# Performance work log

Measured on AMD Instinct MI355X. Metric: run time of the kernel, lower is better.

The kernel has to match this reference:

```python
import jax, jax.numpy as jnp
import numpy as np
from jax import lax

B, T, R, D = 32, 128, 9, 512


def conv2d(x, w, b):
    # x: (N,C,H,W), w: (O,I,kh,kw)
    y = lax.conv_general_dilated(x, w, (1, 1), 'VALID', dimension_numbers=('NCHW', 'OIHW', 'NCHW'))
    return y + b[None, :, None, None]


def pad1(x):
    return jnp.pad(x, ((0, 0), (0, 0), (1, 1), (1, 1)))


def maxpool2(x):
    return lax.reduce_window(x, -jnp.inf, lax.max, (1, 1, 2, 2), (1, 1, 2, 2), 'VALID')


def f2f_similarity(q, t, qm, tm):
    # q,t: (B,T,R,D). Region-pairwise sims then Chamfer: max over target regions p (axis 3), mean over query regions o (axis 2).
    sim = jnp.einsum('biok,bjpk->biopj', q, t)   # (B,T,R,R,T) large intermediate
    sim = jnp.mean(jnp.max(sim, axis=3), axis=2)  # (B,T,T)
    smask = qm[:, :, None] * tm[:, None, :]       # (B,T,T)
    sim = jnp.where(smask > 0, sim, 0.0)
    return sim, smask


def visil_head(sim, mask, w1, b1, w2, b2, w3, b3, wf, bf):
    # ViSiL VideoComperator: zeropad1+conv3x3+relu+maxpool2 (x2), zeropad1+conv3x3+relu, 1x1 conv
    x = sim[:, None]   # (N,1,T,T)
    m = mask[:, None]
    x = maxpool2(jax.nn.relu(conv2d(pad1(x), w1, b1)))
    m = maxpool2(m)
    x = maxpool2(jax.nn.relu(conv2d(pad1(x), w2, b2)))
    m = maxpool2(m)
    x = jax.nn.relu(conv2d(pad1(x), w3, b3))
    x = conv2d(x, wf, bf)   # 1x1 conv -> 1 channel
    return x[:, 0], m[:, 0]


def chamfer_v2v(s, m):
    # masked Chamfer: max over axis 2, masked mean over axis 1
    s = jnp.where(m > 0, s, -jnp.inf)
    s = jnp.max(s, axis=2)
    mm = jnp.max(m, axis=2)
    s = jnp.where(mm > 0, s, 0.0)
    return jnp.sum(s, axis=1) / jnp.sum(mm, axis=1)


def setup_inputs():
    key = jax.random.key(0)
    ks = jax.random.split(key, 8)
    return {
        'anchors': jax.random.normal(ks[0], (B, T, R, D), jnp.float32),
        'positives': jax.random.normal(ks[1], (B, T, R, D), jnp.float32),
        'negatives': jax.random.normal(ks[2], (B, T, R, D), jnp.float32),
        'anchors_masks': jnp.ones((B, T), jnp.float32),
        'positive_masks': jnp.ones((B, T), jnp.float32),
        'negative_masks': jnp.ones((B, T), jnp.float32),
        'w1': jax.random.normal(ks[3], (32, 1, 3, 3), jnp.float32) * 0.05,
        'b1': jnp.zeros((32,), jnp.float32),
        'w2': jax.random.normal(ks[4], (64, 32, 3, 3), jnp.float32) * 0.05,
        'b2': jnp.zeros((64,), jnp.float32),
        'w3': jax.random.normal(ks[5], (128, 64, 3, 3), jnp.float32) * 0.05,
        'b3': jnp.zeros((128,), jnp.float32),
        'wf': jax.random.normal(ks[6], (1, 128, 1, 1), jnp.float32) * 0.05,
        'bf': jnp.zeros((1,), jnp.float32),
    }


def reference(anchors, positives, negatives, anchors_masks, positive_masks, negative_masks, w1, b1, w2, b2, w3, b3, wf, bf):
    pos_sim, pos_mask = f2f_similarity(anchors, positives, anchors_masks, positive_masks)
    neg_sim, neg_mask = f2f_similarity(anchors, negatives, anchors_masks, negative_masks)
    sim = jnp.concatenate([pos_sim, neg_sim], 0)
    smask = jnp.concatenate([pos_mask, neg_mask], 0)
    sim, smask = visil_head(sim, smask, w1, b1, w2, b2, w3, b3, wf, bf)
    # SimilarityRegularizationLoss(min_val=-1, max_val=1)
    loss = jnp.sum(jax.nn.relu(-1.0 - sim)) + jnp.sum(jax.nn.relu(sim - 1.0))
    sim = jnp.clip(sim, -1.0, 1.0)  # Hardtanh
    v2v = chamfer_v2v(sim, smask)   # (2B,)
    pos_pair, neg_pair = jnp.split(v2v[:, None], 2, axis=0)
    return pos_pair, neg_pair, loss
```

## Files before the change

### kernel.cpp

```cpp
#include <hip/hip_runtime.h>
#include <math.h>

#define BTRD (128*9*512)

typedef _Float16 half8 __attribute__((ext_vector_type(8)));
typedef float f32x4 __attribute__((ext_vector_type(4)));

__global__ __launch_bounds__(256) void prep_kernel(
    const float* __restrict__ P, const float* __restrict__ Nn,
    _Float16* __restrict__ Pf, _Float16* __restrict__ Nf,
    const float* __restrict__ w2, const float* __restrict__ w3,
    _Float16* __restrict__ w2t, _Float16* __restrict__ w3t)
{
  int bid = blockIdx.x;
  if (bid < 18432) {
    int which = bid / 9216;
    const float* in = which == 0 ? P : Nn;
    _Float16* out = which == 0 ? Pf : Nf;
    int idx = (bid - which * 9216) * 256 + threadIdx.x;
    const float4* in4 = (const float4*)in;
    float4 a = in4[idx * 2], c = in4[idx * 2 + 1];
    half8 h = { (_Float16)a.x, (_Float16)a.y, (_Float16)a.z, (_Float16)a.w,
                (_Float16)c.x, (_Float16)c.y, (_Float16)c.z, (_Float16)c.w };
    ((half8*)out)[idx] = h;
  } else {
    int idx = (bid - 18432) * 256 + threadIdx.x;
    if (idx < 18432) {
      int tap = idx >> 11, oc = (idx >> 5) & 63, ic = idx & 31;
      w2t[idx] = (_Float16)w2[(oc * 32 + ic) * 9 + tap];
    } else if (idx < 18432 + 73728) {
      int j = idx - 18432;
      int tap = j >> 13, oc = (j >> 6) & 127, ic = j & 63;
      w3t[j] = (_Float16)w3[(oc * 64 + ic) * 9 + tap];
    }
  }
}

template<int O, int OB>
__device__ __forceinline__ void sim_run(
    const float* __restrict__ Q32, const _Float16* __restrict__ TP,
    const _Float16* __restrict__ TN,
    _Float16* __restrict__ lds, int i0, int tid, int jq, int b,
    const float* __restrict__ qm, const float* __restrict__ pm,
    const float* __restrict__ nm, float* __restrict__ simout)
{
  int lane = tid & 63;
  int lrow = lane & 15, lk8 = lane >> 4;
  _Float16* tb0 = lds + 73728;
  _Float16* tb1 = lds + 73728 + 4096;

  {
    const float* qb = Q32 + ((size_t)(i0 * 9) << 9);
#pragma unroll
    for (int it = 0; it < 18; it++) {
      int c = it * 512 + tid;
      int r = c >> 6, sp = c & 63;
      const float* src = qb + ((size_t)r << 9) + (sp << 3);
      float4 a = *(const float4*)src;
      float4 cc = *(const float4*)(src + 4);
      half8 h = { (_Float16)a.x, (_Float16)a.y, (_Float16)a.z, (_Float16)a.w,
                  (_Float16)cc.x, (_Float16)cc.y, (_Float16)cc.z, (_Float16)cc.w };
      *(half8*)&lds[r * 512 + ((sp ^ (r & 7)) << 3)] = h;
    }
  }
  __syncthreads();

  int jc = tid >> 2, spc = tid & 3;
  int ld = jc * 32 + ((spc ^ ((jc >> 1) & 3)) << 3);

  float* ex = (float*)(lds + 73728);
  const float* qmv = qm + b * 128;
  const float inv9 = 1.0f / 9.0f;

  for (int tsel = 0; tsel < 2; ++tsel) {
    const _Float16* tg = (tsel ? TN : TP) + (size_t)jc * 4608 + (spc << 3);

    half8 st[4];
    f32x4 acc[O][2], mx[O][2];
#pragma unroll
    for (int oo = 0; oo < O; oo++)
#pragma unroll
      for (int jt = 0; jt < 2; jt++) {
        acc[oo][jt] = (f32x4){0.f, 0.f, 0.f, 0.f};
        mx[oo][jt] = (f32x4){-INFINITY, -INFINITY, -INFINITY, -INFINITY};
      }

#define T_ISSUE(SET, S) do {                                              \
      int _s = (S);                                                       \
      int _p = _s >> 4; if (_p > 8) _p = 8;                               \
      st[SET] = *(const half8*)(tg + (_p << 9) + ((_s & 15) << 5));       \
    } while (0)

#define T_WRITE(SET, PAR) do {                                            \
      _Float16* _b = (PAR) ? tb1 : tb0;                                   \
      *(half8*)&_b[ld] = st[SET];                                         \
    } while (0)

    T_ISSUE(0, 0);
    T_ISSUE(1, 1);
    T_ISSUE(2, 2);
    T_WRITE(0, 0);
    asm volatile("s_waitcnt lgkmcnt(0)" ::: "memory");
    __builtin_amdgcn_s_barrier();
    __builtin_amdgcn_sched_barrier(0);

    for (int p = 0; p < 9; ++p) {
#pragma unroll
      for (int kc = 0; kc < 16; ++kc) {
        int s = p * 16 + kc;
        T_ISSUE((kc + 3) & 3, s + 3);
        T_WRITE((kc + 1) & 3, (kc + 1) & 1);

        const _Float16* cur = (kc & 1) ? tb1 : tb0;
        half8 bfr[2];
#pragma unroll
        for (int jt = 0; jt < 2; jt++) {
          int j = jq * 32 + jt * 16 + lrow;
          bfr[jt] = *(const half8*)&cur[j * 32 + ((lk8 ^ ((j >> 1) & 3)) << 3)];
        }
#pragma unroll
        for (int oo = 0; oo < O; ++oo) {
          int r = lrow * 9 + OB + oo;
          half8 afr = *(const half8*)&lds[r * 512 + ((((kc << 2) + lk8) ^ (r & 7)) << 3)];
          acc[oo][0] = __builtin_amdgcn_mfma_f32_16x16x32_f16(afr, bfr[0], acc[oo][0], 0, 0, 0);
          acc[oo][1] = __builtin_amdgcn_mfma_f32_16x16x32_f16(afr, bfr[1], acc[oo][1], 0, 0, 0);
        }

        if (kc == 15) {
#pragma unroll
          for (int oo = 0; oo < O; oo++)
#pragma unroll
            for (int jt = 0; jt < 2; jt++) {
#pragma unroll
              for (int e = 0; e < 4; e++)
                mx[oo][jt][e] = fmaxf(mx[oo][jt][e], acc[oo][jt][e]);
              acc[oo][jt] = (f32x4){0.f, 0.f, 0.f, 0.f};
            }
        }
        asm volatile("s_waitcnt lgkmcnt(0)" ::: "memory");
        __builtin_amdgcn_s_barrier();
        __builtin_amdgcn_sched_barrier(0);
      }
    }
#undef T_ISSUE
#undef T_WRITE

    f32x4 ps[2];
#pragma unroll
    for (int jt = 0; jt < 2; jt++) {
      ps[jt] = mx[0][jt];
#pragma unroll
      for (int oo = 1; oo < O; oo++) ps[jt] += mx[oo][jt];
    }

    if (OB != 0) {
#pragma unroll
      for (int jt = 0; jt < 2; jt++)
        *(f32x4*)&ex[((jq * 64 + lane) * 2 + jt) * 4] = ps[jt];
    }
    __syncthreads();
    if (OB == 0) {
      const float* tm = (tsel ? nm : pm) + b * 128;
      int pb = b + tsel * 32;
#pragma unroll
      for (int jt = 0; jt < 2; jt++) {
        ps[jt] += *(const f32x4*)&ex[((jq * 64 + lane) * 2 + jt) * 4];
        int j = jq * 32 + jt * 16 + lrow;
        float tmv = tm[j];
#pragma unroll
        for (int e = 0; e < 4; e++) {
          int i = i0 + (lk8 << 2) + e;
          float m = qmv[i] * tmv;
          simout[((size_t)pb << 14) + (i << 7) + j] = (m > 0.f) ? ps[jt][e] * inv9 : 0.f;
        }
      }
    }
    __syncthreads();
  }
}

__global__ __launch_bounds__(512, 1) void sim_mfma_kernel(
    const float* __restrict__ A32, const _Float16* __restrict__ Pf,
    const _Float16* __restrict__ Nf,
    const float* __restrict__ qm, const float* __restrict__ pm,
    const float* __restrict__ nm, float* __restrict__ simout)
{
  __shared__ _Float16 lds[81920];

  int n = blockIdx.x;
  int xcd = n & 7, slot = n >> 3;
  int b = xcd * 4 + (slot >> 3);
  int ib = slot & 7;
  const float* Q32 = A32 + (size_t)b * BTRD;
  const _Float16* TP = Pf + (size_t)b * BTRD;
  const _Float16* TN = Nf + (size_t)b * BTRD;
  int i0 = ib * 16;

  int tid = threadIdx.x;
  int w = tid >> 6;
  int jq = w & 3;
  if ((w >> 2) == 0)
    sim_run<5, 0>(Q32, TP, TN, lds, i0, tid, jq, b, qm, pm, nm, simout);
  else
    sim_run<4, 5>(Q32, TP, TN, lds, i0, tid, jq, b, qm, pm, nm, simout);
}

__global__ __launch_bounds__(256) void conv1_kernel(
    const float* __restrict__ sim, const float* __restrict__ w1,
    const float* __restrict__ b1, _Float16* __restrict__ x1)
{
  __shared__ float w_s[288];
  __shared__ float b_s[32];
  int tid = threadIdx.x;
  for (int e = tid; e < 288; e += 256) w_s[e] = w1[e];
  if (tid < 32) b_s[tid] = b1[tid];
  __syncthreads();

  int idx = blockIdx.x * 256 + tid;
  int x = idx & 63, y = (idx >> 6) & 63, b2 = idx >> 12;
  const float* sb = sim + (size_t)b2 * 16384;

  float patch[4][4];
#pragma unroll
  for (int r = 0; r < 4; r++) {
    int Y = 2 * y - 1 + r;
#pragma unroll
    for (int c = 0; c < 4; c++) {
      int X = 2 * x - 1 + c;
      patch[r][c] = (Y >= 0 && Y < 128 && X >= 0 && X < 128) ? sb[Y * 128 + X] : 0.f;
    }
  }

  _Float16 vout[32];
#pragma unroll
  for (int oc = 0; oc < 32; oc++) {
    float c00 = 0, c01 = 0, c10 = 0, c11 = 0;
#pragma unroll
    for (int tap = 0; tap < 9; tap++) {
      int dy = tap / 3, dx = tap - dy * 3;
      float w = w_s[oc * 9 + tap];
      c00 = fmaf(w, patch[dy][dx], c00);
      c01 = fmaf(w, patch[dy][dx + 1], c01);
      c10 = fmaf(w, patch[dy + 1][dx], c10);
      c11 = fmaf(w, patch[dy + 1][dx + 1], c11);
    }
    float v = fmaxf(fmaxf(c00, c01), fmaxf(c10, c11)) + b_s[oc];
    vout[oc] = (_Float16)fmaxf(v, 0.f);
  }
  _Float16* dst = x1 + (((size_t)b2 * 64 + y) * 64 + x) * 32;
#pragma unroll
  for (int q = 0; q < 4; q++)
    *(half8*)(dst + q * 8) = *(half8*)&vout[q * 8];
}

__global__ __launch_bounds__(256, 2) void conv2_mfma(
    const _Float16* __restrict__ x1, const _Float16* __restrict__ w2t,
    const float* __restrict__ bb, _Float16* __restrict__ x2)
{
  __shared__ _Float16 in_s[4 * 6 * 66 * 8];
  __shared__ _Float16 w_s[9 * 64 * 40];
  __shared__ _Float16 pool_s[4][32 * 32];

  int b2 = blockIdx.y, ystrip = blockIdx.x;
  int y0 = ystrip * 4;
  int tid = threadIdx.x;
  int w = tid >> 6, lane = tid & 63;
  int wyp = w >> 1, wn = w & 1;
  int lrow = lane & 15, lk8 = lane >> 4;

  {
    int px = tid >> 2, seg = tid & 3;
    const _Float16* base = x1 + ((size_t)b2 * 64) * 64 * 32;
    for (int rr = 0; rr < 6; rr++) {
      int yy = y0 - 1 + rr;
      half8 v = {};
      if (yy >= 0 && yy < 64) v = *(const half8*)(base + ((size_t)yy * 64 + px) * 32 + seg * 8);
      *(half8*)&in_s[((seg * 6 + rr) * 66 + px + 1) * 8] = v;
    }
    if (tid < 48) {
      int pr = tid >> 1, side = tid & 1;
      *(half8*)&in_s[(pr * 66 + side * 65) * 8] = (half8){};
    }
  }
  for (int e = tid; e < 2304; e += 256)
    *(half8*)&w_s[(e >> 2) * 40 + (e & 3) * 8] = *(const half8*)&w2t[e * 8];
  __syncthreads();

  f32x4 acc[2][4][2];
#pragma unroll
  for (int yr = 0; yr < 2; yr++)
#pragma unroll
    for (int xt = 0; xt < 4; xt++)
#pragma unroll
      for (int nt = 0; nt < 2; nt++)
        acc[yr][xt][nt] = (f32x4){0.f, 0.f, 0.f, 0.f};

#pragma unroll
  for (int tap = 0; tap < 9; tap++) {
    int dy = tap / 3, dx = tap - dy * 3;
    half8 bfr[2];
#pragma unroll
    for (int nt = 0; nt < 2; nt++)
      bfr[nt] = *(const half8*)&w_s[(tap * 64 + wn * 32 + nt * 16 + lrow) * 40 + lk8 * 8];
#pragma unroll
    for (int yr = 0; yr < 2; yr++) {
      int rr = 2 * wyp + yr + dy;
#pragma unroll
      for (int xt = 0; xt < 4; xt++) {
        half8 afr = *(const half8*)&in_s[((lk8 * 6 + rr) * 66 + xt * 16 + lrow + dx) * 8];
#pragma unroll
        for (int nt = 0; nt < 2; nt++)
          acc[yr][xt][nt] = __builtin_amdgcn_mfma_f32_16x16x32_f16(afr, bfr[nt], acc[yr][xt][nt], 0, 0, 0);
      }
    }
  }

  float bbv[2] = { bb[wn * 32 + lrow], bb[wn * 32 + 16 + lrow] };
#pragma unroll
  for (int nt = 0; nt < 2; nt++)
#pragma unroll
    for (int xt = 0; xt < 4; xt++)
#pragma unroll
      for (int pe = 0; pe < 2; pe++) {
        float m = fmaxf(fmaxf(acc[0][xt][nt][2 * pe], acc[0][xt][nt][2 * pe + 1]),
                        fmaxf(acc[1][xt][nt][2 * pe], acc[1][xt][nt][2 * pe + 1]));
        float v = fmaxf(m + bbv[nt], 0.f);
        int px = xt * 8 + lk8 * 2 + pe;
        pool_s[w][px * 32 + nt * 16 + lrow] = (_Float16)v;
      }
  __syncthreads();

  {
    int py = ystrip * 2 + wyp;
    int px = lane & 31, half = lane >> 5;
    const _Float16* srcp = &pool_s[w][px * 32 + half * 16];
    _Float16* dst = x2 + (((size_t)b2 * 32 + py) * 32 + px) * 64 + wn * 32 + half * 16;
    *(half8*)dst = *(const half8*)srcp;
    *(half8*)(dst + 8) = *(const half8*)(srcp + 8);
  }
}

__global__ __launch_bounds__(256, 2) void conv3_mfma(
    const _Float16* __restrict__ x2, const _Float16* __restrict__ w3t,
    const float* __restrict__ b3, const float* __restrict__ wf,
    const float* __restrict__ bf, float* __restrict__ shead)
{
  __shared__ _Float16 in_s[8 * 6 * 34 * 8];
  __shared__ _Float16 w_s[9 * 32 * 72];

  int b2 = blockIdx.y, ystrip = blockIdx.x;
  int y0 = ystrip * 4;
  int tid = threadIdx.x, w = tid >> 6, lane = tid & 63;
  int lrow = lane & 15, lk8 = lane >> 4;

  {
    int px = tid >> 3, seg = tid & 7;
    const _Float16* base = x2 + ((size_t)b2 * 32) * 32 * 64;
    for (int rr = 0; rr < 6; rr++) {
      int yy = y0 - 1 + rr;
      half8 v = {};
      if (yy >= 0 && yy < 32) v = *(const half8*)(base + ((size_t)yy * 32 + px) * 64 + seg * 8);
      *(half8*)&in_s[((seg * 6 + rr) * 34 + px + 1) * 8] = v;
    }
    if (tid < 96) {
      int pr = tid >> 1, side = tid & 1;
      *(half8*)&in_s[(pr * 34 + side * 33) * 8] = (half8){};
    }
  }

  f32x4 spart[2];
  spart[0] = (f32x4){0.f, 0.f, 0.f, 0.f};
  spart[1] = (f32x4){0.f, 0.f, 0.f, 0.f};
  int y = y0 + w;

  for (int og = 0; og < 4; og++) {
    __syncthreads();
    for (int e = tid; e < 2304; e += 256) {
      int s = e & 7, o = (e >> 3) & 31, tap = e >> 8;
      *(half8*)&w_s[(tap * 32 + o) * 72 + s * 8] =
          *(const half8*)&w3t[((size_t)(tap * 128 + og * 32 + o)) * 64 + s * 8];
    }
    __syncthreads();

    f32x4 acc[2][2];
#pragma unroll
    for (int mt = 0; mt < 2; mt++)
#pragma unroll
      for (int nt = 0; nt < 2; nt++)
        acc[mt][nt] = (f32x4){0.f, 0.f, 0.f, 0.f};

#pragma unroll
    for (int tap = 0; tap < 9; tap++) {
      int dy = tap / 3, dx = tap - dy * 3;
#pragma unroll
      for (int kc = 0; kc < 2; kc++) {
        half8 bfr[2];
#pragma unroll
        for (int nt = 0; nt < 2; nt++)
          bfr[nt] = *(const half8*)&w_s[(tap * 32 + nt * 16 + lrow) * 72 + kc * 32 + lk8 * 8];
#pragma unroll
        for (int mt = 0; mt < 2; mt++) {
          half8 afr = *(const half8*)&in_s[(((kc * 4 + lk8) * 6 + w + dy) * 34 + mt * 16 + lrow + dx) * 8];
#pragma unroll
          for (int nt = 0; nt < 2; nt++)
            acc[mt][nt] = __builtin_amdgcn_mfma_f32_16x16x32_f16(afr, bfr[nt], acc[mt][nt], 0, 0, 0);
        }
      }
    }

#pragma unroll
    for (int nt = 0; nt < 2; nt++) {
      int oc = og * 32 + nt * 16 + lrow;
      float b3v = b3[oc], wfv = wf[oc];
#pragma unroll
      for (int mt = 0; mt < 2; mt++)
#pragma unroll
        for (int e = 0; e < 4; e++)
          spart[mt][e] = fmaf(fmaxf(acc[mt][nt][e] + b3v, 0.f), wfv, spart[mt][e]);
    }
  }

#pragma unroll
  for (int mt = 0; mt < 2; mt++)
#pragma unroll
    for (int e = 0; e < 4; e++) {
      float v = spart[mt][e];
      v += __shfl_xor(v, 1); v += __shfl_xor(v, 2);
      v += __shfl_xor(v, 4); v += __shfl_xor(v, 8);
      spart[mt][e] = v;
    }
  if (lrow == 0) {
    float bfv = bf[0];
#pragma unroll
    for (int mt = 0; mt < 2; mt++)
#pragma unroll
      for (int e = 0; e < 4; e++) {
        int x = mt * 16 + lk8 * 4 + e;
        shead[(size_t)b2 * 1024 + y * 32 + x] = spart[mt][e] + bfv;
      }
  }
}

__global__ __launch_bounds__(256) void head_final_kernel(
    const float* __restrict__ shead, const float* __restrict__ qm,
    const float* __restrict__ pm, const float* __restrict__ nm,
    float* __restrict__ out, float* __restrict__ loss_ws)
{
  int b2 = blockIdx.x, b = b2 & 31, g = b2 >> 5;
  const float* qmv = qm + b * 128;
  const float* tmv = (g ? nm : pm) + b * 128;

  __shared__ float mq4[32], mt4[32];
  __shared__ float red[256];
  __shared__ float rowv[32], rowm[32];

  int tid = threadIdx.x;
  if (tid < 32) {
    float a = qmv[tid * 4];
    a = fmaxf(a, qmv[tid * 4 + 1]); a = fmaxf(a, qmv[tid * 4 + 2]); a = fmaxf(a, qmv[tid * 4 + 3]);
    mq4[tid] = a;
    float c = tmv[tid * 4];
    c = fmaxf(c, tmv[tid * 4 + 1]); c = fmaxf(c, tmv[tid * 4 + 2]); c = fmaxf(c, tmv[tid * 4 + 3]);
    mt4[tid] = c;
  }
  __syncthreads();

  const float* s = shead + (size_t)b2 * 1024;
  float lp = 0.f;
#pragma unroll
  for (int r = 0; r < 4; r++) {
    float v = s[tid + 256 * r];
    lp += fmaxf(-1.f - v, 0.f) + fmaxf(v - 1.f, 0.f);
  }
  red[tid] = lp;
  __syncthreads();
  for (int off = 128; off; off >>= 1) {
    if (tid < off) red[tid] += red[tid + off];
    __syncthreads();
  }
  if (tid == 0) loss_ws[b2] = red[0];

  if (tid < 32) {
    int y = tid;
    float mqy = mq4[y];
    float rmax = -INFINITY, mm = 0.f;
    for (int x = 0; x < 32; x++) {
      float m = mqy * mt4[x];
      mm = fmaxf(mm, m);
      float v = s[y * 32 + x];
      v = fminf(fmaxf(v, -1.f), 1.f);
      rmax = fmaxf(rmax, m > 0.f ? v : -INFINITY);
    }
    rowv[y] = (mm > 0.f) ? rmax : 0.f;
    rowm[y] = mm;
  }
  __syncthreads();
  if (tid == 0) {
    float ss = 0.f, sm = 0.f;
    for (int y = 0; y < 32; y++) { ss += rowv[y]; sm += rowm[y]; }
    out[b2] = ss / sm;
  }
}

__global__ void loss_sum_kernel(const float* __restrict__ loss_ws, float* __restrict__ out)
{
  float v = loss_ws[threadIdx.x];
#pragma unroll
  for (int off = 32; off >= 1; off >>= 1) v += __shfl_down(v, off);
  if (threadIdx.x == 0) out[64] = v;
}

extern "C" void kernel_launch(void* const* d_in, const int* in_sizes, int n_in,
                              void* d_out, int out_size, void* d_ws, size_t ws_size,
                              hipStream_t stream)
{
  (void)in_sizes; (void)n_in; (void)out_size; (void)ws_size;
  const float* A   = (const float*)d_in[0];
  const float* P   = (const float*)d_in[1];
  const float* Nn  = (const float*)d_in[2];
  const float* qm  = (const float*)d_in[3];
  const float* pm  = (const float*)d_in[4];
  const float* nm  = (const float*)d_in[5];
  const float* w1  = (const float*)d_in[6];
  const float* b1  = (const float*)d_in[7];
  const float* w2  = (const float*)d_in[8];
  const float* b2w = (const float*)d_in[9];
  const float* w3  = (const float*)d_in[10];
  const float* b3  = (const float*)d_in[11];
  const float* wf  = (const float*)d_in[12];
  const float* bf  = (const float*)d_in[13];
  float* out = (float*)d_out;

  const size_t F16SZ = (size_t)BTRD * 32 * sizeof(_Float16);
  char* ws = (char*)d_ws;
  _Float16* Pf = (_Float16*)(ws);
  _Float16* Nf = (_Float16*)(ws + F16SZ);
  char* ws2 = ws + 2 * F16SZ;
  float*     sim   = (float*)(ws2);
  _Float16*  x1    = (_Float16*)(ws2 + (4u << 20));
  _Float16*  x2    = (_Float16*)(ws2 + (20u << 20));
  float*     shead = (float*)(ws2 + (28u << 20));
  _Float16*  w2t   = (_Float16*)(ws2 + (29u << 20));
  _Float16*  w3t   = (_Float16*)(ws2 + (29u << 20) + (256u << 10));
  float*     lws   = (float*)(ws2 + (30u << 20));

  prep_kernel<<<18792, 256, 0, stream>>>(P, Nn, Pf, Nf, w2, w3, w2t, w3t);

  sim_mfma_kernel<<<256, 512, 0, stream>>>(A, Pf, Nf, qm, pm, nm, sim);
  conv1_kernel<<<1024, 256, 0, stream>>>(sim, w1, b1, x1);
  conv2_mfma<<<dim3(16, 64), 256, 0, stream>>>(x1, w2t, b2w, x2);
  conv3_mfma<<<dim3(8, 64), 256, 0, stream>>>(x2, w3t, b3, wf, bf, shead);
  head_final_kernel<<<64, 256, 0, stream>>>(shead, qm, pm, nm, out, lws);
  loss_sum_kernel<<<1, 64, 0, stream>>>(lws, out);
}
```

Measured before the change: 202.1 us.

## Fuse fp32-to-fp16 conversion of targets into sim kernel and prioritize MFMA waves

Removes the separate prep pass that converted the positive and negative tensors to fp16 in workspace. The sim kernel now loads fp32 target tiles straight from the inputs and converts them to fp16 while staging into LDS. This drops a full read-convert-write round trip over both tensors but doubles the global bytes each sim block loads for targets and adds register pressure. It also raises wave priority with s_setprio around the MFMA section.

```diff
diff --git a/kernel.cpp b/kernel.cpp
--- a/kernel.cpp
+++ b/kernel.cpp
@@ -7,39 +7,24 @@
 typedef float f32x4 __attribute__((ext_vector_type(4)));
 
 __global__ __launch_bounds__(256) void prep_kernel(
-    const float* __restrict__ P, const float* __restrict__ Nn,
-    _Float16* __restrict__ Pf, _Float16* __restrict__ Nf,
     const float* __restrict__ w2, const float* __restrict__ w3,
     _Float16* __restrict__ w2t, _Float16* __restrict__ w3t)
 {
-  int bid = blockIdx.x;
-  if (bid < 18432) {
-    int which = bid / 9216;
-    const float* in = which == 0 ? P : Nn;
-    _Float16* out = which == 0 ? Pf : Nf;
-    int idx = (bid - which * 9216) * 256 + threadIdx.x;
-    const float4* in4 = (const float4*)in;
-    float4 a = in4[idx * 2], c = in4[idx * 2 + 1];
-    half8 h = { (_Float16)a.x, (_Float16)a.y, (_Float16)a.z, (_Float16)a.w,
-                (_Float16)c.x, (_Float16)c.y, (_Float16)c.z, (_Float16)c.w };
-    ((half8*)out)[idx] = h;
-  } else {
-    int idx = (bid - 18432) * 256 + threadIdx.x;
-    if (idx < 18432) {
-      int tap = idx >> 11, oc = (idx >> 5) & 63, ic = idx & 31;
-      w2t[idx] = (_Float16)w2[(oc * 32 + ic) * 9 + tap];
-    } else if (idx < 18432 + 73728) {
-      int j = idx - 18432;
-      int tap = j >> 13, oc = (j >> 6) & 127, ic = j & 63;
-      w3t[j] = (_Float16)w3[(oc * 64 + ic) * 9 + tap];
-    }
+  int idx = blockIdx.x * 256 + threadIdx.x;
+  if (idx < 18432) {
+    int tap = idx >> 11, oc = (idx >> 5) & 63, ic = idx & 31;
+    w2t[idx] = (_Float16)w2[(oc * 32 + ic) * 9 + tap];
+  } else if (idx < 18432 + 73728) {
+    int j = idx - 18432;
+    int tap = j >> 13, oc = (j >> 6) & 127, ic = j & 63;
+    w3t[j] = (_Float16)w3[(oc * 64 + ic) * 9 + tap];
   }
 }
 
 template<int O, int OB>
 __device__ __forceinline__ void sim_run(
-    const float* __restrict__ Q32, const _Float16* __restrict__ TP,
-    const _Float16* __restrict__ TN,
+    const float* __restrict__ Q32, const float* __restrict__ TP,
+    const float* __restrict__ TN,
     _Float16* __restrict__ lds, int i0, int tid, int jq, int b,
     const float* __restrict__ qm, const float* __restrict__ pm,
     const float* __restrict__ nm, float* __restrict__ simout)
@@ -73,9 +58,9 @@
   const float inv9 = 1.0f / 9.0f;
 
   for (int tsel = 0; tsel < 2; ++tsel) {
-    const _Float16* tg = (tsel ? TN : TP) + (size_t)jc * 4608 + (spc << 3);
-
-    half8 st[4];
+    const float* tg = (tsel ? TN : TP) + (size_t)jc * 4608 + (spc << 3);
+
+    float4 sta[4], stb[4];
     f32x4 acc[O][2], mx[O][2];
 #pragma unroll
     for (int oo = 0; oo < O; oo++)
@@ -88,12 +73,18 @@
 #define T_ISSUE(SET, S) do {                                              \
       int _s = (S);                                                       \
       int _p = _s >> 4; if (_p > 8) _p = 8;                               \
-      st[SET] = *(const half8*)(tg + (_p << 9) + ((_s & 15) << 5));       \
+      const float* _src = tg + (_p << 9) + ((_s & 15) << 5);              \
+      sta[SET] = *(const float4*)_src;                                    \
+      stb[SET] = *(const float4*)(_src + 4);                              \
     } while (0)
 
 #define T_WRITE(SET, PAR) do {                                            \
       _Float16* _b = (PAR) ? tb1 : tb0;                                   \
-      *(half8*)&_b[ld] = st[SET];                                         \
+      half8 _h = { (_Float16)sta[SET].x, (_Float16)sta[SET].y,            \
+                   (_Float16)sta[SET].z, (_Float16)sta[SET].w,            \
+                   (_Float16)stb[SET].x, (_Float16)stb[SET].y,            \
+                   (_Float16)stb[SET].z, (_Float16)stb[SET].w };          \
+      *(half8*)&_b[ld] = _h;                                              \
     } while (0)
 
     T_ISSUE(0, 0);
@@ -118,6 +109,7 @@
           int j = jq * 32 + jt * 16 + lrow;
           bfr[jt] = *(const half8*)&cur[j * 32 + ((lk8 ^ ((j >> 1) & 3)) << 3)];
         }
+        __builtin_amdgcn_s_setprio(1);
 #pragma unroll
         for (int oo = 0; oo < O; ++oo) {
           int r = lrow * 9 + OB + oo;
@@ -125,6 +117,7 @@
           acc[oo][0] = __builtin_amdgcn_mfma_f32_16x16x32_f16(afr, bfr[0], acc[oo][0], 0, 0, 0);
           acc[oo][1] = __builtin_amdgcn_mfma_f32_16x16x32_f16(afr, bfr[1], acc[oo][1], 0, 0, 0);
         }
+        __builtin_amdgcn_s_setprio(0);
 
         if (kc == 15) {
 #pragma unroll
@@ -180,8 +173,8 @@
 }
 
 __global__ __launch_bounds__(512, 1) void sim_mfma_kernel(
-    const float* __restrict__ A32, const _Float16* __restrict__ Pf,
-    const _Float16* __restrict__ Nf,
+    const float* __restrict__ A32, const float* __restrict__ P32,
+    const float* __restrict__ N32,
     const float* __restrict__ qm, const float* __restrict__ pm,
     const float* __restrict__ nm, float* __restrict__ simout)
 {
@@ -192,8 +185,8 @@
   int b = xcd * 4 + (slot >> 3);
   int ib = slot & 7;
   const float* Q32 = A32 + (size_t)b * BTRD;
-  const _Float16* TP = Pf + (size_t)b * BTRD;
-  const _Float16* TN = Nf + (size_t)b * BTRD;
+  const float* TP = P32 + (size_t)b * BTRD;
+  const float* TN = N32 + (size_t)b * BTRD;
   int i0 = ib * 16;
 
   int tid = threadIdx.x;
@@ -531,22 +524,18 @@
   const float* bf  = (const float*)d_in[13];
   float* out = (float*)d_out;
 
-  const size_t F16SZ = (size_t)BTRD * 32 * sizeof(_Float16);
   char* ws = (char*)d_ws;
-  _Float16* Pf = (_Float16*)(ws);
-  _Float16* Nf = (_Float16*)(ws + F16SZ);
-  char* ws2 = ws + 2 * F16SZ;
-  float*     sim   = (float*)(ws2);
-  _Float16*  x1    = (_Float16*)(ws2 + (4u << 20));
-  _Float16*  x2    = (_Float16*)(ws2 + (20u << 20));
-  float*     shead = (float*)(ws2 + (28u << 20));
-  _Float16*  w2t   = (_Float16*)(ws2 + (29u << 20));
-  _Float16*  w3t   = (_Float16*)(ws2 + (29u << 20) + (256u << 10));
-  float*     lws   = (float*)(ws2 + (30u << 20));
-
-  prep_kernel<<<18792, 256, 0, stream>>>(P, Nn, Pf, Nf, w2, w3, w2t, w3t);
-
-  sim_mfma_kernel<<<256, 512, 0, stream>>>(A, Pf, Nf, qm, pm, nm, sim);
+  float*     sim   = (float*)(ws);
+  _Float16*  x1    = (_Float16*)(ws + (4u << 20));
+  _Float16*  x2    = (_Float16*)(ws + (20u << 20));
+  float*     shead = (float*)(ws + (28u << 20));
+  _Float16*  w2t   = (_Float16*)(ws + (29u << 20));
+  _Float16*  w3t   = (_Float16*)(ws + (29u << 20) + (256u << 10));
+  float*     lws   = (float*)(ws + (30u << 20));
+
+  prep_kernel<<<360, 256, 0, stream>>>(w2, w3, w2t, w3t);
+
+  sim_mfma_kernel<<<256, 512, 0, stream>>>(A, P, Nn, qm, pm, nm, sim);
   conv1_kernel<<<1024, 256, 0, stream>>>(sim, w1, b1, x1);
   conv2_mfma<<<dim3(16, 64), 256, 0, stream>>>(x1, w2t, b2w, x2);
   conv3_mfma<<<dim3(8, 64), 256, 0, stream>>>(x2, w3t, b3, wf, bf, shead);
```

Result: slower. 290.3 us (+43.6%).

## Stream target tiles directly to LDS with global_load_lds double buffering

Applied to the files above, without the earlier changes.

Replaces the register-staged global-load-then-LDS-store pipeline for target tiles with direct global-to-LDS loads (global_load_lds, 16 bytes), moving the swizzle into the global source address. Each step issues the next tile and waits with vmcnt(1), bracketed by two barriers. This drops register staging and the separate ds_write, but shortens the prefetch distance from three stages to one and adds an extra barrier per step, so global latency may be less hidden.

```diff
diff --git a/kernel.cpp b/kernel.cpp
--- a/kernel.cpp
+++ b/kernel.cpp
@@ -5,6 +5,12 @@
 
 typedef _Float16 half8 __attribute__((ext_vector_type(8)));
 typedef float f32x4 __attribute__((ext_vector_type(4)));
+
+__device__ __forceinline__ void gload16(const _Float16* g, const _Float16* l) {
+  __builtin_amdgcn_global_load_lds(
+      (const __attribute__((address_space(1))) void*)g,
+      (__attribute__((address_space(3))) void*)l, 16, 0, 0);
+}
 
 __global__ __launch_bounds__(256) void prep_kernel(
     const float* __restrict__ P, const float* __restrict__ Nn,
@@ -66,16 +72,16 @@
   __syncthreads();
 
   int jc = tid >> 2, spc = tid & 3;
-  int ld = jc * 32 + ((spc ^ ((jc >> 1) & 3)) << 3);
+  int spl = spc ^ ((jc >> 1) & 3);
+  int wb8 = (tid & ~63) * 8;
 
   float* ex = (float*)(lds + 73728);
   const float* qmv = qm + b * 128;
   const float inv9 = 1.0f / 9.0f;
 
   for (int tsel = 0; tsel < 2; ++tsel) {
-    const _Float16* tg = (tsel ? TN : TP) + (size_t)jc * 4608 + (spc << 3);
-
-    half8 st[4];
+    const _Float16* tg = (tsel ? TN : TP) + (size_t)jc * 4608 + (spl << 3);
+
     f32x4 acc[O][2], mx[O][2];
 #pragma unroll
     for (int oo = 0; oo < O; oo++)
@@ -85,31 +91,28 @@
         mx[oo][jt] = (f32x4){-INFINITY, -INFINITY, -INFINITY, -INFINITY};
       }
 
-#define T_ISSUE(SET, S) do {                                              \
+#define T_ISSUE_G(S) do {                                                 \
       int _s = (S);                                                       \
-      int _p = _s >> 4; if (_p > 8) _p = 8;                               \
-      st[SET] = *(const half8*)(tg + (_p << 9) + ((_s & 15) << 5));       \
+      int _p = _s >> 4;                                                   \
+      _Float16* _buf = ((_s) & 1) ? tb1 : tb0;                            \
+      gload16(tg + (_p << 9) + ((_s & 15) << 5), _buf + wb8);             \
     } while (0)
 
-#define T_WRITE(SET, PAR) do {                                            \
-      _Float16* _b = (PAR) ? tb1 : tb0;                                   \
-      *(half8*)&_b[ld] = st[SET];                                         \
-    } while (0)
-
-    T_ISSUE(0, 0);
-    T_ISSUE(1, 1);
-    T_ISSUE(2, 2);
-    T_WRITE(0, 0);
-    asm volatile("s_waitcnt lgkmcnt(0)" ::: "memory");
-    __builtin_amdgcn_s_barrier();
-    __builtin_amdgcn_sched_barrier(0);
+    T_ISSUE_G(0);
 
     for (int p = 0; p < 9; ++p) {
 #pragma unroll
       for (int kc = 0; kc < 16; ++kc) {
         int s = p * 16 + kc;
-        T_ISSUE((kc + 3) & 3, s + 3);
-        T_WRITE((kc + 1) & 3, (kc + 1) & 1);
+        __builtin_amdgcn_s_barrier();
+        if (s < 143) {
+          T_ISSUE_G(s + 1);
+          asm volatile("s_waitcnt vmcnt(1)" ::: "memory");
+        } else {
+          asm volatile("s_waitcnt vmcnt(0)" ::: "memory");
+        }
+        __builtin_amdgcn_s_barrier();
+        __builtin_amdgcn_sched_barrier(0);
 
         const _Float16* cur = (kc & 1) ? tb1 : tb0;
         half8 bfr[2];
@@ -137,13 +140,9 @@
               acc[oo][jt] = (f32x4){0.f, 0.f, 0.f, 0.f};
             }
         }
-        asm volatile("s_waitcnt lgkmcnt(0)" ::: "memory");
-        __builtin_amdgcn_s_barrier();
-        __builtin_amdgcn_sched_barrier(0);
-      }
-    }
-#undef T_ISSUE
-#undef T_WRITE
+      }
+    }
+#undef T_ISSUE_G
 
     f32x4 ps[2];
 #pragma unroll
@@ -153,6 +152,7 @@
       for (int oo = 1; oo < O; oo++) ps[jt] += mx[oo][jt];
     }
 
+    __syncthreads();
     if (OB != 0) {
 #pragma unroll
       for (int jt = 0; jt < 2; jt++)
```

Result: faster. 191.5 us (-5.2%).

## Give each wave a private LDS target tile and drop per-step block barriers

Applied to the files above, without the earlier changes.

Previously all four waves cooperatively staged target chunks into a shared double-buffered LDS tile, with a block-wide barrier after every k-step. Now each wave loads the 32 target rows it needs into its own single-buffered LDS slice, so the per-step s_barrier and waitcnt go away. Within a wave, LDS reads and writes stay in order, so one buffer is enough. The cost is duplicated global/L2 loads, since waves sharing the same jq now fetch the same rows, plus twice as many loads per thread. A __syncthreads is added before the cross-wave exchange because that exchange area overlaps the private slices.

```diff
diff --git a/kernel.cpp b/kernel.cpp
--- a/kernel.cpp
+++ b/kernel.cpp
@@ -46,8 +46,8 @@
 {
   int lane = tid & 63;
   int lrow = lane & 15, lk8 = lane >> 4;
-  _Float16* tb0 = lds + 73728;
-  _Float16* tb1 = lds + 73728 + 4096;
+  int w = tid >> 6;
+  _Float16* priv = lds + 73728 + w * 1024;
 
   {
     const float* qb = Q32 + ((size_t)(i0 * 9) << 9);
@@ -65,17 +65,21 @@
   }
   __syncthreads();
 
-  int jc = tid >> 2, spc = tid & 3;
-  int ld = jc * 32 + ((spc ^ ((jc >> 1) & 3)) << 3);
+  int j0l = lane >> 2, s0 = lane & 3;
+  int j1l = j0l + 16;
+  int ld0 = j0l * 32 + ((s0 ^ ((j0l >> 1) & 3)) << 3);
+  int ld1 = j1l * 32 + ((s0 ^ ((j1l >> 1) & 3)) << 3);
 
   float* ex = (float*)(lds + 73728);
   const float* qmv = qm + b * 128;
   const float inv9 = 1.0f / 9.0f;
 
   for (int tsel = 0; tsel < 2; ++tsel) {
-    const _Float16* tg = (tsel ? TN : TP) + (size_t)jc * 4608 + (spc << 3);
-
-    half8 st[4];
+    const _Float16* tg0 = (tsel ? TN : TP) +
+        (size_t)(jq * 32 + j0l) * 4608 + (s0 << 3);
+    const _Float16* tg1 = tg0 + (size_t)16 * 4608;
+
+    half8 st[4][2];
     f32x4 acc[O][2], mx[O][2];
 #pragma unroll
     for (int oo = 0; oo < O; oo++)
@@ -88,36 +92,34 @@
 #define T_ISSUE(SET, S) do {                                              \
       int _s = (S);                                                       \
       int _p = _s >> 4; if (_p > 8) _p = 8;                               \
-      st[SET] = *(const half8*)(tg + (_p << 9) + ((_s & 15) << 5));       \
+      int _off = (_p << 9) + ((_s & 15) << 5);                            \
+      st[SET][0] = *(const half8*)(tg0 + _off);                           \
+      st[SET][1] = *(const half8*)(tg1 + _off);                           \
     } while (0)
 
-#define T_WRITE(SET, PAR) do {                                            \
-      _Float16* _b = (PAR) ? tb1 : tb0;                                   \
-      *(half8*)&_b[ld] = st[SET];                                         \
+#define T_WRITE(SET) do {                                                 \
+      *(half8*)&priv[ld0] = st[SET][0];                                   \
+      *(half8*)&priv[ld1] = st[SET][1];                                   \
     } while (0)
 
     T_ISSUE(0, 0);
     T_ISSUE(1, 1);
     T_ISSUE(2, 2);
-    T_WRITE(0, 0);
-    asm volatile("s_waitcnt lgkmcnt(0)" ::: "memory");
-    __builtin_amdgcn_s_barrier();
-    __builtin_amdgcn_sched_barrier(0);
+    T_WRITE(0);
 
     for (int p = 0; p < 9; ++p) {
 #pragma unroll
       for (int kc = 0; kc < 16; ++kc) {
         int s = p * 16 + kc;
+        half8 bfr[2];
+#pragma unroll
+        for (int jt = 0; jt < 2; jt++) {
+          int jl = jt * 16 + lrow;
+          bfr[jt] = *(const half8*)&priv[jl * 32 + ((lk8 ^ ((jl >> 1) & 3)) << 3)];
+        }
         T_ISSUE((kc + 3) & 3, s + 3);
-        T_WRITE((kc + 1) & 3, (kc + 1) & 1);
-
-        const _Float16* cur = (kc & 1) ? tb1 : tb0;
-        half8 bfr[2];
-#pragma unroll
-        for (int jt = 0; jt < 2; jt++) {
-          int j = jq * 32 + jt * 16 + lrow;
-          bfr[jt] = *(const half8*)&cur[j * 32 + ((lk8 ^ ((j >> 1) & 3)) << 3)];
-        }
+        T_WRITE((kc + 1) & 3);
+
 #pragma unroll
         for (int oo = 0; oo < O; ++oo) {
           int r = lrow * 9 + OB + oo;
@@ -137,9 +139,6 @@
               acc[oo][jt] = (f32x4){0.f, 0.f, 0.f, 0.f};
             }
         }
-        asm volatile("s_waitcnt lgkmcnt(0)" ::: "memory");
-        __builtin_amdgcn_s_barrier();
-        __builtin_amdgcn_sched_barrier(0);
       }
     }
 #undef T_ISSUE
@@ -153,6 +152,7 @@
       for (int oo = 1; oo < O; oo++) ps[jt] += mx[oo][jt];
     }
 
+    __syncthreads();
     if (OB != 0) {
 #pragma unroll
       for (int jt = 0; jt < 2; jt++)
```

Result: slower. 206.9 us (+2.4%).
